# Optimization experiments

Measured on AMD Instinct MI355X. Metric: run time of the kernel, lower is better.

The kernel has to match this reference:

```python
import jax, jax.numpy as jnp
import numpy as np

B, S, D = 4, 4096, 1024
DD = 4 * D
N_EXPERTS = 8
CAPACITY = 1.0
LN_EPS = 1e-5


def setup_inputs() -> dict:
    key = jax.random.key(0)
    ks = jax.random.split(key, 8)
    s1 = 1.0 / np.sqrt(D)
    s2 = 1.0 / np.sqrt(DD)
    return {
        "x": jax.random.normal(ks[0], (B, S, D), jnp.float32),
        "gate_w": jax.random.normal(ks[1], (N_EXPERTS, D), jnp.float32) * 0.02,
        "ln_w": jnp.ones((D,), jnp.float32),
        "ln_b": jnp.zeros((D,), jnp.float32),
        "fc1s": jax.random.normal(ks[2], (N_EXPERTS, DD, D), jnp.float32) * s1,
        "b1s": jax.random.normal(ks[3], (N_EXPERTS, DD), jnp.float32) * s1,
        "fc2s": jax.random.normal(ks[4], (N_EXPERTS, D, DD), jnp.float32) * s2,
        "b2s": jax.random.normal(ks[5], (N_EXPERTS, D), jnp.float32) * s2,
    }


def reference(x, gate_w, ln_w, ln_b, fc1s, b1s, fc2s, b2s):
    og_shape = x.shape
    d = og_shape[-1]
    xf = x.reshape(-1, d)                       # (bs, d)
    bs = xf.shape[0]
    n = gate_w.shape[0]
    k = int(bs * CAPACITY) // n                 # static capacity per expert

    # softmax gating over experts
    scores = jax.nn.softmax(xf @ gate_w.T, axis=-1)   # (bs, n)

    # per-expert top-k tokens (column-wise descending sort, take first k)
    vals, idx = jax.lax.top_k(scores.T, k)      # (n, k)
    kept_w = vals.T                              # (k, n)
    kept_idx = idx.T                             # (k, n)
    flat_idx = kept_idx.reshape(-1)              # (k*n,) row-major: k outer, n inner

    # gather selected tokens, layernorm
    y = xf[flat_idx].reshape(k, n, d)            # (k, n, d)
    mu = y.mean(-1, keepdims=True)
    var = ((y - mu) ** 2).mean(-1, keepdims=True)
    y = (y - mu) * jax.lax.rsqrt(var + LN_EPS) * ln_w + ln_b

    # per-expert grouped GEMMs
    h = jnp.einsum('knd,nfd->knf', y, fc1s) + b1s          # (k, n, dd)
    h = jax.nn.gelu(h, approximate=True)                   # tanh gelu
    out = jnp.einsum('knf,ndf->knd', h, fc2s) + b2s        # (k, n, d)

    # weight by gate scores and scatter-add back onto the input tokens
    out = out * kept_w[..., None]
    xf = xf.at[flat_idx].add(out.reshape(k * n, d))
    return xf.reshape(og_shape)
```

## Files before the change

### kernel.cpp

```cpp
#include <hip/hip_runtime.h>

#define TOK  16384
#define NEXP 8
#define DIM  1024
#define DDIM 4096
#define KCAP 2048

typedef float  floatx4 __attribute__((ext_vector_type(4)));
typedef short  shortx8 __attribute__((ext_vector_type(8)));

static __device__ __forceinline__ unsigned short f2bf(float x) {
  unsigned u = __float_as_uint(x);
  return (unsigned short)((u + 0x7fffu + ((u >> 16) & 1u)) >> 16);
}

__global__ __launch_bounds__(256) void cvt_kernel(const float* __restrict__ src,
                                                  unsigned short* __restrict__ dst, int n4) {
  int i = blockIdx.x * 256 + threadIdx.x;
  if (i < n4) {
    float4 v = ((const float4*)src)[i];
    ushort4 o = make_ushort4(f2bf(v.x), f2bf(v.y), f2bf(v.z), f2bf(v.w));
    ((ushort4*)dst)[i] = o;
  }
}

__global__ __launch_bounds__(256) void gate_kernel(const float* __restrict__ x,
                                                   const float* __restrict__ gw,
                                                   float* __restrict__ scores) {
  __shared__ float gws[NEXP * DIM];
  int tid = threadIdx.x;
  for (int i = tid; i < NEXP * DIM / 4; i += 256)
    ((float4*)gws)[i] = ((const float4*)gw)[i];
  __syncthreads();
  int wave = tid >> 6, lane = tid & 63;
  int t = blockIdx.x * 4 + wave;
  const float4* xr = (const float4*)(x + (size_t)t * DIM);
  float4 xv[4];
#pragma unroll
  for (int j = 0; j < 4; ++j) xv[j] = xr[j * 64 + lane];
  float acc[NEXP];
#pragma unroll
  for (int e = 0; e < NEXP; ++e) acc[e] = 0.f;
#pragma unroll
  for (int e = 0; e < NEXP; ++e) {
    const float4* g4 = (const float4*)(gws + e * DIM);
#pragma unroll
    for (int j = 0; j < 4; ++j) {
      float4 g = g4[j * 64 + lane];
      acc[e] += xv[j].x * g.x + xv[j].y * g.y + xv[j].z * g.z + xv[j].w * g.w;
    }
  }
#pragma unroll
  for (int off = 32; off > 0; off >>= 1) {
#pragma unroll
    for (int e = 0; e < NEXP; ++e) acc[e] += __shfl_down(acc[e], off);
  }
  if (lane == 0) {
    float mx = acc[0];
#pragma unroll
    for (int e = 1; e < NEXP; ++e) mx = fmaxf(mx, acc[e]);
    float ex[NEXP], sum = 0.f;
#pragma unroll
    for (int e = 0; e < NEXP; ++e) { ex[e] = expf(acc[e] - mx); sum += ex[e]; }
    float inv = 1.f / sum;
#pragma unroll
    for (int e = 0; e < NEXP; ++e) scores[(size_t)e * TOK + t] = ex[e] * inv;
  }
}

#define TKT 1024
#define TKW (TKT / 64)
__global__ __launch_bounds__(TKT) void topk_kernel(const float* __restrict__ scores,
                                                   int* __restrict__ sel,
                                                   float* __restrict__ selw) {
  int e = blockIdx.x;
  const float* s = scores + (size_t)e * TOK;
  int tid = threadIdx.x, lane = tid & 63, wave = tid >> 6;
  __shared__ int cnt;
  __shared__ int wsum[TKW];

  unsigned prefix = 0;
  for (int bit = 30; bit >= 0; --bit) {
    unsigned cand = prefix | (1u << bit);
    if (tid == 0) cnt = 0;
    __syncthreads();
    int c = 0;
    for (int i = tid; i < TOK; i += TKT) c += (__float_as_uint(s[i]) >= cand) ? 1 : 0;
#pragma unroll
    for (int off = 32; off > 0; off >>= 1) c += __shfl_down(c, off);
    if (lane == 0) atomicAdd(&cnt, c);
    __syncthreads();
    if (cnt >= KCAP) prefix = cand;
    __syncthreads();
  }
  unsigned T = prefix;

  if (tid == 0) cnt = 0;
  __syncthreads();
  {
    int c = 0;
    for (int i = tid; i < TOK; i += TKT) c += (__float_as_uint(s[i]) > T) ? 1 : 0;
#pragma unroll
    for (int off = 32; off > 0; off >>= 1) c += __shfl_down(c, off);
    if (lane == 0) atomicAdd(&cnt, c);
  }
  __syncthreads();
  int n_gt = cnt;
  int need = KCAP - n_gt;

  __shared__ int pos;
  __shared__ int tiebase;
  if (tid == 0) { pos = 0; tiebase = 0; }
  __syncthreads();
  for (int chunk = 0; chunk < TOK; chunk += TKT) {
    int i = chunk + tid;
    unsigned v = __float_as_uint(s[i]);
    if (v > T) {
      int p = atomicAdd(&pos, 1);
      sel[e * KCAP + p]  = i;
      selw[e * KCAP + p] = __uint_as_float(v);
    }
    bool tie = (v == T);
    unsigned long long m = __ballot(tie);
    if (lane == 0) wsum[wave] = __popcll(m);
    __syncthreads();
    int base = tiebase;
    for (int w = 0; w < wave; ++w) base += wsum[w];
    int rank = base + __popcll(m & ((1ull << lane) - 1ull));
    if (tie && rank < need) {
      sel[e * KCAP + n_gt + rank]  = i;
      selw[e * KCAP + n_gt + rank] = __uint_as_float(T);
    }
    __syncthreads();
    if (tid == 0) {
      int tb = 0;
#pragma unroll
      for (int w = 0; w < TKW; ++w) tb += wsum[w];
      tiebase += tb;
    }
    __syncthreads();
  }
}

__global__ __launch_bounds__(256) void gather_ln_kernel(const float* __restrict__ x,
                                                        const int* __restrict__ sel,
                                                        const float* __restrict__ lnw,
                                                        const float* __restrict__ lnb,
                                                        unsigned short* __restrict__ Y) {
  int e = blockIdx.y, i = blockIdx.x;
  int tid = threadIdx.x, lane = tid & 63, wave = tid >> 6;
  int t = sel[e * KCAP + i];
  const float4* xr = (const float4*)(x + (size_t)t * DIM);
  float4 v = xr[tid];
  float s  = v.x + v.y + v.z + v.w;
  float sq = v.x * v.x + v.y * v.y + v.z * v.z + v.w * v.w;
#pragma unroll
  for (int off = 32; off > 0; off >>= 1) { s += __shfl_down(s, off); sq += __shfl_down(sq, off); }
  __shared__ float red[8];
  if (lane == 0) { red[wave] = s; red[4 + wave] = sq; }
  __syncthreads();
  s  = red[0] + red[1] + red[2] + red[3];
  sq = red[4] + red[5] + red[6] + red[7];
  float mu  = s * (1.f / DIM);
  float var = sq * (1.f / DIM) - mu * mu;
  float rs  = rsqrtf(var + 1e-5f);
  float4 w = ((const float4*)lnw)[tid];
  float4 b = ((const float4*)lnb)[tid];
  ushort4 o = make_ushort4(f2bf((v.x - mu) * rs * w.x + b.x),
                           f2bf((v.y - mu) * rs * w.y + b.y),
                           f2bf((v.z - mu) * rs * w.z + b.z),
                           f2bf((v.w - mu) * rs * w.w + b.w));
  ((ushort4*)(Y + ((size_t)e * KCAP + i) * DIM))[tid] = o;
}

#define BM  256
#define BN  256
#define BKT 64
#define HTILE 8192

template <int MODE>
__global__ __launch_bounds__(512, 2) void gemm_kernel(
    const unsigned short* __restrict__ Aall,
    const unsigned short* __restrict__ Ball,
    const float* __restrict__ biasAll,
    int M, int N, int K,
    unsigned short* __restrict__ Hall,
    float* __restrict__ Out,
    const int* __restrict__ sel, const float* __restrict__ selw) {

  __shared__ __align__(16) unsigned short As[2 * 2 * HTILE];
  __shared__ __align__(16) unsigned short Bs[2 * 2 * HTILE];
  __shared__ int   selS[BM];
  __shared__ float wS[BM];

  int tid = threadIdx.x, lane = tid & 63, wave = tid >> 6;
  int m_w = wave >> 2, n_w = wave & 3;
  int hb  = n_w >> 1, nb0 = (n_w & 1) * 64;
  int row = lane & 15, quad = lane >> 4, r7 = row & 7;
  int r8 = lane >> 3, j8 = lane & 7;

  int nxt = N >> 8, nyt = M >> 8, per = nxt * nyt;
  int nwg = per * NEXP;
  int bid = blockIdx.x;
  int swz = (bid & 7) * (nwg >> 3) + (bid >> 3);
  int e   = swz / per;
  int rem = swz - e * per;
  int by  = rem / nxt;
  int bx  = rem - by * nxt;
  int m0 = by * BM, n0 = bx * BN;
  int NT = K / BKT;

  const unsigned short* A = Aall + (size_t)e * M * K;
  const unsigned short* B = Ball + (size_t)e * N * K;
  const float* bias = biasAll + (size_t)e * N;

  if (MODE == 2 && tid < BM) {
    selS[tid] = sel[e * KCAP + m0 + tid];
    wS[tid]   = selw[e * KCAP + m0 + tid];
  }
  __syncthreads();

#define STAGE(DST, G, RC0, TT, HALF, BUF)                                              \
  do {                                                                                 \
    int tt_ = (TT) < NT ? (TT) : NT - 1;                                               \
    const unsigned short* g_ =                                                         \
        (G) + (size_t)((RC0) + (HALF) * 128 + wave * 16 + r8) * K + tt_ * BKT +        \
        ((j8 ^ r8) << 3);                                                              \
    unsigned short* l_ = (DST) + ((BUF) * 2 + (HALF)) * HTILE + wave * 16 * 64;        \
    __builtin_amdgcn_global_load_lds((const __attribute__((address_space(1))) void*)g_,\
        (__attribute__((address_space(3))) void*)l_, 16, 0, 0);                        \
    __builtin_amdgcn_global_load_lds(                                                  \
        (const __attribute__((address_space(1))) void*)(g_ + (size_t)8 * K),           \
        (__attribute__((address_space(3))) void*)(l_ + 8 * 64), 16, 0, 0);             \
  } while (0)

#define LDA(MQ)                                                                        \
  _Pragma("unroll") for (int ti = 0; ti < 4; ++ti)                                     \
  _Pragma("unroll") for (int kki = 0; kki < 2; ++kki)                                  \
    a[ti][kki] = *(const shortx8*)&As[(cur * 2 + m_w) * HTILE +                        \
        ((MQ) * 64 + ti * 16 + row) * 64 + (((quad + 4 * kki) ^ r7) << 3)];

#define LDB(BREG, NQ)                                                                  \
  _Pragma("unroll") for (int tj = 0; tj < 2; ++tj)                                     \
  _Pragma("unroll") for (int kki = 0; kki < 2; ++kki)                                  \
    BREG[tj][kki] = *(const shortx8*)&Bs[(cur * 2 + hb) * HTILE +                      \
        (nb0 + (NQ) * 32 + tj * 16 + row) * 64 + (((quad + 4 * kki) ^ r7) << 3)];

#define MFMAQ(MQ, BREG, NQ)                                                            \
  _Pragma("unroll") for (int ti = 0; ti < 4; ++ti)                                     \
  _Pragma("unroll") for (int tj = 0; tj < 2; ++tj)                                     \
  _Pragma("unroll") for (int kki = 0; kki < 2; ++kki)                                  \
    acc[(MQ) * 4 + ti][(NQ) * 2 + tj] = __builtin_amdgcn_mfma_f32_16x16x32_bf16(       \
        a[ti][kki], BREG[tj][kki], acc[(MQ) * 4 + ti][(NQ) * 2 + tj], 0, 0, 0);

#define PH_MID()                                                                       \
  __builtin_amdgcn_s_barrier();                                                        \
  asm volatile("s_waitcnt lgkmcnt(0)" ::: "memory");                                   \
  __builtin_amdgcn_s_setprio(1);

#define PH_END()                                                                       \
  __builtin_amdgcn_s_setprio(0);                                                       \
  __builtin_amdgcn_s_barrier();

#define PH_END_VM()                                                                    \
  __builtin_amdgcn_s_setprio(0);                                                       \
  asm volatile("s_waitcnt vmcnt(2)" ::: "memory");                                     \
  __builtin_amdgcn_s_barrier();

  floatx4 acc[8][4];
  floatx4 zero = {0.f, 0.f, 0.f, 0.f};
#pragma unroll
  for (int i = 0; i < 8; ++i)
#pragma unroll
    for (int j = 0; j < 4; ++j) acc[i][j] = zero;

  shortx8 a[4][2], b0[2][2], b1[2][2];

  STAGE(As, A, m0, 0, 0, 0);
  STAGE(As, A, m0, 0, 1, 0);
  STAGE(Bs, B, n0, 0, 0, 0);
  STAGE(Bs, B, n0, 0, 1, 0);
  STAGE(As, A, m0, 1, 0, 1);
  asm volatile("s_waitcnt vmcnt(2)" ::: "memory");
  __builtin_amdgcn_s_barrier();

  for (int t = 0; t < NT; ++t) {
    int cur = t & 1, nb = cur ^ 1;
    LDA(0); LDB(b0, 0);
    STAGE(As, A, m0, t + 1, 1, nb);
    asm volatile("s_waitcnt lgkmcnt(8)" ::: "memory");
    PH_MID(); MFMAQ(0, b0, 0); PH_END();
    LDB(b1, 1);
    STAGE(Bs, B, n0, t + 1, 0, nb);
    PH_MID(); MFMAQ(0, b1, 1); PH_END();
    LDA(1);
    STAGE(Bs, B, n0, t + 1, 1, nb);
    PH_MID(); MFMAQ(1, b0, 0); PH_END();
    STAGE(As, A, m0, t + 2, 0, cur);
    PH_MID(); MFMAQ(1, b1, 1); PH_END_VM();
  }

#pragma unroll
  for (int ti = 0; ti < 8; ++ti) {
#pragma unroll
    for (int tj = 0; tj < 4; ++tj) {
      int gn = n0 + n_w * 64 + tj * 16 + row;
      float bb = bias[gn];
#pragma unroll
      for (int r = 0; r < 4; ++r) {
        int lrow = m_w * 128 + ti * 16 + quad * 4 + r;
        float v = acc[ti][tj][r] + bb;
        if (MODE == 1) {
          float u = 0.7978845608028654f * (v + 0.044715f * v * v * v);
          u = fminf(u, 15.f);
          float e2 = __expf(2.f * u);
          float th = __fdividef(e2 - 1.f, e2 + 1.f);
          float g = 0.5f * v * (1.f + th);
          Hall[(size_t)e * M * N + (size_t)(m0 + lrow) * N + gn] = f2bf(g);
        } else {
          atomicAdd(&Out[(size_t)selS[lrow] * DIM + gn], wS[lrow] * v);
        }
      }
    }
  }
#undef STAGE
#undef LDA
#undef LDB
#undef MFMAQ
#undef PH_MID
#undef PH_END
#undef PH_END_VM
}

extern "C" void kernel_launch(void* const* d_in, const int* in_sizes, int n_in,
                              void* d_out, int out_size, void* d_ws, size_t ws_size,
                              hipStream_t stream) {
  const float* x   = (const float*)d_in[0];
  const float* gw  = (const float*)d_in[1];
  const float* lnw = (const float*)d_in[2];
  const float* lnb = (const float*)d_in[3];
  const float* fc1 = (const float*)d_in[4];
  const float* b1  = (const float*)d_in[5];
  const float* fc2 = (const float*)d_in[6];
  const float* b2  = (const float*)d_in[7];
  float* out = (float*)d_out;

  char* p = (char*)d_ws;
  float* scores = (float*)p;                 p += (size_t)NEXP * TOK * 4;
  int*   sel    = (int*)p;                   p += (size_t)NEXP * KCAP * 4;
  float* selw   = (float*)p;                 p += (size_t)NEXP * KCAP * 4;
  unsigned short* Wb = (unsigned short*)p;   p += (size_t)NEXP * DDIM * DIM * 2;
  unsigned short* Y  = (unsigned short*)p;   p += (size_t)NEXP * KCAP * DIM * 2;
  unsigned short* H  = (unsigned short*)p;   p += (size_t)NEXP * KCAP * DDIM * 2;

  hipMemcpyAsync(out, x, (size_t)TOK * DIM * sizeof(float), hipMemcpyDeviceToDevice, stream);

  gate_kernel<<<TOK / 4, 256, 0, stream>>>(x, gw, scores);
  topk_kernel<<<NEXP, TKT, 0, stream>>>(scores, sel, selw);
  gather_ln_kernel<<<dim3(KCAP, NEXP), 256, 0, stream>>>(x, sel, lnw, lnb, Y);

  const int n4w = NEXP * DDIM * DIM / 4;
  cvt_kernel<<<n4w / 256, 256, 0, stream>>>(fc1, Wb, n4w);
  gemm_kernel<1><<<dim3((DDIM / BN) * (KCAP / BM) * NEXP), 512, 0, stream>>>(
      Y, Wb, b1, KCAP, DDIM, DIM, H, nullptr, nullptr, nullptr);

  cvt_kernel<<<n4w / 256, 256, 0, stream>>>(fc2, Wb, n4w);
  gemm_kernel<2><<<dim3((DIM / BN) * (KCAP / BM) * NEXP), 512, 0, stream>>>(
      H, Wb, b2, KCAP, DIM, DDIM, nullptr, out, sel, selw);
}
```

Before: 780.2 us.

## Use radix-histogram top-k threshold and retune GEMM prefetch schedule

```diff
diff --git a/kernel.cpp b/kernel.cpp
--- a/kernel.cpp
+++ b/kernel.cpp
@@ -70,42 +70,78 @@
 
 #define TKT 1024
 #define TKW (TKT / 64)
+
+__device__ __forceinline__ void walk_suffix(const int* hist, int nbins, int cnt_in,
+                                            int tid, int* shOut) {
+  if (tid < 64) {
+    int lane = tid;
+    int cum = 0;
+    for (int g = nbins / 64 - 1; g >= 0; --g) {
+      int c = hist[g * 64 + lane];
+      int s = c;
+#pragma unroll
+      for (int off = 1; off < 64; off <<= 1) {
+        int o = __shfl_down(s, off);
+        if (lane + off < 64) s += o;
+      }
+      int gs = __shfl(s, 0);
+      if (cnt_in + cum + gs >= KCAP) {
+        unsigned long long m = __ballot(cnt_in + cum + s >= KCAP);
+        int l = 63 - __clzll(m);
+        int sAt = __shfl(s, l), cAt = __shfl(c, l);
+        if (lane == 0) { shOut[0] = g * 64 + l; shOut[1] = cnt_in + cum + sAt - cAt; }
+        break;
+      }
+      cum += gs;
+    }
+  }
+}
+
 __global__ __launch_bounds__(TKT) void topk_kernel(const float* __restrict__ scores,
                                                    int* __restrict__ sel,
                                                    float* __restrict__ selw) {
   int e = blockIdx.x;
   const float* s = scores + (size_t)e * TOK;
   int tid = threadIdx.x, lane = tid & 63, wave = tid >> 6;
-  __shared__ int cnt;
+  __shared__ int hist[2048];
+  __shared__ int shBin[2];
   __shared__ int wsum[TKW];
 
-  unsigned prefix = 0;
-  for (int bit = 30; bit >= 0; --bit) {
-    unsigned cand = prefix | (1u << bit);
-    if (tid == 0) cnt = 0;
-    __syncthreads();
-    int c = 0;
-    for (int i = tid; i < TOK; i += TKT) c += (__float_as_uint(s[i]) >= cand) ? 1 : 0;
-#pragma unroll
-    for (int off = 32; off > 0; off >>= 1) c += __shfl_down(c, off);
-    if (lane == 0) atomicAdd(&cnt, c);
-    __syncthreads();
-    if (cnt >= KCAP) prefix = cand;
-    __syncthreads();
-  }
-  unsigned T = prefix;
-
-  if (tid == 0) cnt = 0;
-  __syncthreads();
-  {
-    int c = 0;
-    for (int i = tid; i < TOK; i += TKT) c += (__float_as_uint(s[i]) > T) ? 1 : 0;
-#pragma unroll
-    for (int off = 32; off > 0; off >>= 1) c += __shfl_down(c, off);
-    if (lane == 0) atomicAdd(&cnt, c);
-  }
-  __syncthreads();
-  int n_gt = cnt;
+  for (int i = tid; i < 2048; i += TKT) hist[i] = 0;
+  __syncthreads();
+  for (int i = tid; i < TOK; i += TKT)
+    atomicAdd(&hist[__float_as_uint(s[i]) >> 21], 1);
+  __syncthreads();
+  walk_suffix(hist, 2048, 0, tid, shBin);
+  __syncthreads();
+  unsigned bin1 = (unsigned)shBin[0];
+  int cab = shBin[1];
+  __syncthreads();
+
+  for (int i = tid; i < 2048; i += TKT) hist[i] = 0;
+  __syncthreads();
+  for (int i = tid; i < TOK; i += TKT) {
+    unsigned v = __float_as_uint(s[i]);
+    if ((v >> 21) == bin1) atomicAdd(&hist[(v >> 10) & 0x7FFu], 1);
+  }
+  __syncthreads();
+  walk_suffix(hist, 2048, cab, tid, shBin);
+  __syncthreads();
+  unsigned pre21 = (bin1 << 11) | (unsigned)shBin[0];
+  cab = shBin[1];
+  __syncthreads();
+
+  for (int i = tid; i < 1024; i += TKT) hist[i] = 0;
+  __syncthreads();
+  for (int i = tid; i < TOK; i += TKT) {
+    unsigned v = __float_as_uint(s[i]);
+    if ((v >> 10) == pre21) atomicAdd(&hist[v & 0x3FFu], 1);
+  }
+  __syncthreads();
+  walk_suffix(hist, 1024, cab, tid, shBin);
+  __syncthreads();
+  unsigned T = (pre21 << 10) | (unsigned)shBin[0];
+  int n_gt = shBin[1];
   int need = KCAP - n_gt;
 
   __shared__ int pos;
@@ -178,12 +214,11 @@
 #define BKT 64
 #define HTILE 8192
 
-template <int MODE>
+template <int MODE, int M, int N, int K>
 __global__ __launch_bounds__(512, 2) void gemm_kernel(
     const unsigned short* __restrict__ Aall,
     const unsigned short* __restrict__ Ball,
     const float* __restrict__ biasAll,
-    int M, int N, int K,
     unsigned short* __restrict__ Hall,
     float* __restrict__ Out,
     const int* __restrict__ sel, const float* __restrict__ selw) {
@@ -199,8 +234,8 @@
   int row = lane & 15, quad = lane >> 4, r7 = row & 7;
   int r8 = lane >> 3, j8 = lane & 7;
 
-  int nxt = N >> 8, nyt = M >> 8, per = nxt * nyt;
-  int nwg = per * NEXP;
+  constexpr int nxt = N >> 8, nyt = M >> 8, per = nxt * nyt;
+  constexpr int nwg = per * NEXP;
   int bid = blockIdx.x;
   int swz = (bid & 7) * (nwg >> 3) + (bid >> 3);
   int e   = swz / per;
@@ -208,7 +243,7 @@
   int by  = rem / nxt;
   int bx  = rem - by * nxt;
   int m0 = by * BM, n0 = bx * BN;
-  int NT = K / BKT;
+  constexpr int NT = K / BKT;
 
   const unsigned short* A = Aall + (size_t)e * M * K;
   const unsigned short* B = Ball + (size_t)e * N * K;
@@ -247,9 +282,9 @@
         (nb0 + (NQ) * 32 + tj * 16 + row) * 64 + (((quad + 4 * kki) ^ r7) << 3)];
 
 #define MFMAQ(MQ, BREG, NQ)                                                            \
+  _Pragma("unroll") for (int kki = 0; kki < 2; ++kki)                                  \
   _Pragma("unroll") for (int ti = 0; ti < 4; ++ti)                                     \
   _Pragma("unroll") for (int tj = 0; tj < 2; ++tj)                                     \
-  _Pragma("unroll") for (int kki = 0; kki < 2; ++kki)                                  \
     acc[(MQ) * 4 + ti][(NQ) * 2 + tj] = __builtin_amdgcn_mfma_f32_16x16x32_bf16(       \
         a[ti][kki], BREG[tj][kki], acc[(MQ) * 4 + ti][(NQ) * 2 + tj], 0, 0, 0);
 
@@ -262,9 +297,9 @@
   __builtin_amdgcn_s_setprio(0);                                                       \
   __builtin_amdgcn_s_barrier();
 
-#define PH_END_VM()                                                                    \
+#define PH_END_VM(NN)                                                                  \
   __builtin_amdgcn_s_setprio(0);                                                       \
-  asm volatile("s_waitcnt vmcnt(2)" ::: "memory");                                     \
+  asm volatile("s_waitcnt vmcnt(" #NN ")" ::: "memory");                               \
   __builtin_amdgcn_s_barrier();
 
   floatx4 acc[8][4];
@@ -277,28 +312,30 @@
   shortx8 a[4][2], b0[2][2], b1[2][2];
 
   STAGE(As, A, m0, 0, 0, 0);
+  STAGE(Bs, B, n0, 0, 0, 0);
   STAGE(As, A, m0, 0, 1, 0);
-  STAGE(Bs, B, n0, 0, 0, 0);
   STAGE(Bs, B, n0, 0, 1, 0);
   STAGE(As, A, m0, 1, 0, 1);
-  asm volatile("s_waitcnt vmcnt(2)" ::: "memory");
+  STAGE(Bs, B, n0, 1, 0, 1);
+  asm volatile("s_waitcnt vmcnt(4)" ::: "memory");
   __builtin_amdgcn_s_barrier();
 
   for (int t = 0; t < NT; ++t) {
     int cur = t & 1, nb = cur ^ 1;
     LDA(0); LDB(b0, 0);
     STAGE(As, A, m0, t + 1, 1, nb);
+    STAGE(Bs, B, n0, t + 1, 1, nb);
     asm volatile("s_waitcnt lgkmcnt(8)" ::: "memory");
     PH_MID(); MFMAQ(0, b0, 0); PH_END();
     LDB(b1, 1);
-    STAGE(Bs, B, n0, t + 1, 0, nb);
     PH_MID(); MFMAQ(0, b1, 1); PH_END();
     LDA(1);
-    STAGE(Bs, B, n0, t + 1, 1, nb);
     PH_MID(); MFMAQ(1, b0, 0); PH_END();
     STAGE(As, A, m0, t + 2, 0, cur);
-    PH_MID(); MFMAQ(1, b1, 1); PH_END_VM();
-  }
+    STAGE(Bs, B, n0, t + 2, 0, cur);
+    PH_MID(); MFMAQ(1, b1, 1); PH_END_VM(4);
+  }
+  asm volatile("s_waitcnt vmcnt(0)" ::: "memory");
 
 #pragma unroll
   for (int ti = 0; ti < 8; ++ti) {
@@ -361,10 +398,10 @@
 
   const int n4w = NEXP * DDIM * DIM / 4;
   cvt_kernel<<<n4w / 256, 256, 0, stream>>>(fc1, Wb, n4w);
-  gemm_kernel<1><<<dim3((DDIM / BN) * (KCAP / BM) * NEXP), 512, 0, stream>>>(
-      Y, Wb, b1, KCAP, DDIM, DIM, H, nullptr, nullptr, nullptr);
+  gemm_kernel<1, KCAP, DDIM, DIM><<<dim3((DDIM / BN) * (KCAP / BM) * NEXP), 512, 0, stream>>>(
+      Y, Wb, b1, H, nullptr, nullptr, nullptr);
 
   cvt_kernel<<<n4w / 256, 256, 0, stream>>>(fc2, Wb, n4w);
-  gemm_kernel<2><<<dim3((DIM / BN) * (KCAP / BM) * NEXP), 512, 0, stream>>>(
-      H, Wb, b2, KCAP, DIM, DDIM, nullptr, out, sel, selw);
-}
+  gemm_kernel<2, KCAP, DIM, DDIM><<<dim3((DIM / BN) * (KCAP / BM) * NEXP), 512, 0, stream>>>(
+      H, Wb, b2, nullptr, out, sel, selw);
+}
```

After: 826.8 us. 1.06x slower.
